# Performance work log

Hardware: AMD Instinct MI355X
Metric: run time of the kernel (lower is better)

The kernel has to match this reference:

```python
import jax, jax.numpy as jnp
import numpy as np

B, S, H = 4, 256, 768
F = 32            # num_features
T = 256           # TAG_HIDDEN_SIZE
WD = 64           # WIDTH_HIDDEN_SIZE
C = 16            # num_tags


def setup_inputs() -> dict:
    key = jax.random.key(0)
    ks = jax.random.split(key, 10)
    inp = {
        "final_hidden": jax.random.normal(ks[0], (B, S, H), jnp.float32),
        "feature_vecs": jax.random.normal(ks[1], (B, S, F), jnp.float32),
        # Linear params stored [in, out] (transposed vs torch; same math)
        "start_W": jax.random.normal(ks[2], (H + F, T), jnp.float32) * (1.0 / np.sqrt(H + F)),
        "start_b": jnp.zeros((T,), jnp.float32),
        "end_W": jax.random.normal(ks[3], (H + F, T), jnp.float32) * (1.0 / np.sqrt(H + F)),
        "end_b": jnp.zeros((T,), jnp.float32),
        "U": jax.random.normal(ks[4], (T, C, T), jnp.float32) * (1.0 / np.sqrt(T)),
        "width_hidden": jax.random.uniform(ks[5], (S, S, WD), jnp.float32),
        "lin_W": jax.random.normal(ks[6], (2 * T + WD, C), jnp.float32) * (1.0 / np.sqrt(2 * T + WD)),
        "lin_b": jnp.zeros((C,), jnp.float32),
    }
    return inp


def reference(final_hidden, feature_vecs, start_W, start_b, end_W, end_b, U, width_hidden, lin_W, lin_b):
    # dropout p=0.0 -> identity
    x = jnp.concatenate([final_hidden, feature_vecs], axis=-1)   # [B,S,H+F]
    s = x @ start_W + start_b                                    # [B,S,T]
    e = x @ end_W + end_b                                        # [B,S,T]

    # biaffine term: einsum('bsh,hci->bsci') then ('bsci,bei->bsec')
    sU = jnp.einsum('bst,tcu->bscu', s, U)                       # [B,S,C,T]
    pre = jnp.einsum('bscu,beu->bsec', sU, e)                    # [B,S,S,C]

    # pairwise FFN, fused: Linear over concat(start, end, width) decomposes
    # into three small matmuls + broadcast adds (same math, no O(S^2*(2T+W)) buffer)
    Ws, We, Ww = lin_W[:T], lin_W[T:2 * T], lin_W[2 * T:]
    ffn = (jnp.einsum('bst,tc->bsc', s, Ws)[:, :, None, :]
           + jnp.einsum('bet,tc->bec', e, We)[:, None, :, :]
           + jnp.einsum('sew,wc->sec', width_hidden, Ww)[None]
           + lin_b)                                              # [B,S,S,C]
    return pre + ffn
```

## Files before the change

kernel.cpp:

```cpp
#include <hip/hip_runtime.h>


#define B_ 4
#define S_ 256
#define H_ 768
#define F_ 32
#define T_ 256
#define C_ 16
#define R_ 1024
#define HF 800
#define HFP 832

typedef unsigned short u16;
typedef __attribute__((ext_vector_type(8))) short short8;
typedef __attribute__((ext_vector_type(4))) float f32x4;

__device__ __forceinline__ u16 f2b(float x) {
    unsigned u = __builtin_bit_cast(unsigned, x);
    u += 0x7FFF + ((u >> 16) & 1);
    return (u16)(u >> 16);
}
__device__ __forceinline__ float b2f(u16 b) {
    unsigned u = ((unsigned)b) << 16;
    return __builtin_bit_cast(float, u);
}

template<int K, int LDA, int LDB, int MF, int NF, int UNROLL>
__device__ __forceinline__ void core(const u16* __restrict__ A,
                                     const u16* __restrict__ B,
                                     int lr, int kgl, f32x4 acc[MF][NF])
{
    const u16* ap[MF];
    const u16* bp[NF];
#pragma unroll
    for (int i = 0; i < MF; ++i) ap[i] = A + (size_t)(i * 16 + lr) * LDA + kgl * 8;
#pragma unroll
    for (int j = 0; j < NF; ++j) bp[j] = B + (size_t)(j * 16 + lr) * LDB + kgl * 8;

#pragma unroll UNROLL
    for (int k = 0; k < K; k += 32) {
        short8 a[MF], b[NF];
#pragma unroll
        for (int i = 0; i < MF; ++i) a[i] = *(const short8*)(ap[i] + k);
#pragma unroll
        for (int j = 0; j < NF; ++j) b[j] = *(const short8*)(bp[j] + k);
#pragma unroll
        for (int i = 0; i < MF; ++i)
#pragma unroll
            for (int j = 0; j < NF; ++j)
                acc[i][j] = __builtin_amdgcn_mfma_f32_16x16x32_bf16(a[i], b[j], acc[i][j], 0, 0, 0);
    }
}

__global__ __launch_bounds__(256)
void k_cvt1(const float* __restrict__ fh, const float* __restrict__ fv,
            const float* __restrict__ sW, const float* __restrict__ eW,
            u16* __restrict__ Xb, u16* __restrict__ Wt)
{
    const int bid = blockIdx.x;
    const int tid = threadIdx.x;

    if (bid < 832) {
        int idx = bid * 256 + tid;
        int r = idx / 208, c4 = idx % 208;
        int k = c4 * 4;
        float4 v;
        if (k < H_)       v = *(const float4*)&fh[r * H_ + k];
        else if (k < HF)  v = *(const float4*)&fv[r * F_ + k - H_];
        else              v = make_float4(0.f, 0.f, 0.f, 0.f);
        ushort4 o; o.x = f2b(v.x); o.y = f2b(v.y); o.z = f2b(v.z); o.w = f2b(v.w);
        *(ushort4*)&Xb[(size_t)r * HFP + k] = o;
    } else if (bid < 1232) {
        __shared__ float t_[32][33];
        int bid2 = bid - 832;
        int k0 = (bid2 / 16) * 32;
        int j0 = (bid2 % 16) * 32;
        const float* src = (j0 < T_) ? sW : eW;
        const int js = (j0 < T_) ? j0 : j0 - T_;
        {
            int jl = tid & 31, kl0 = (tid >> 5) * 4;
#pragma unroll
            for (int i = 0; i < 4; ++i)
                t_[kl0 + i][jl] = src[(k0 + kl0 + i) * T_ + js + jl];
        }
        __syncthreads();
        {
            int kl = tid & 31, jl0 = (tid >> 5) * 4;
#pragma unroll
            for (int i = 0; i < 4; ++i)
                Wt[(size_t)(j0 + jl0 + i) * HFP + k0 + kl] = f2b(t_[kl][jl0 + i]);
        }
    } else {
        int idx = (bid - 1232) * 256 + tid;
        int r = idx >> 3, c4 = idx & 7;
        ushort4 z; z.x = z.y = z.z = z.w = 0;
        *(ushort4*)&Wt[(size_t)r * HFP + HF + c4 * 4] = z;
    }
}

__global__ __launch_bounds__(256)
void k_se_cvtu(const u16* __restrict__ Xb, const u16* __restrict__ Wt,
               const float* __restrict__ sb, const float* __restrict__ eb,
               const float* __restrict__ U,
               u16* __restrict__ SEb, u16* __restrict__ Ut)
{
    const int bid = blockIdx.x;
    const int tid = threadIdx.x;

    if (bid < 256) {
        const int l = tid & 63, w = tid >> 6;
        const int wj = w & 1, wr2 = w >> 1;
        const int lr = l & 15, kgl = l >> 4;
        const int bm = (bid & 15) * 32;
        const int bn = (bid >> 4) * 64;
        f32x4 acc[1][2] = {};

        core<HFP, HFP, HFP, 1, 2, 2>(Wt + (size_t)(bm + wj * 16) * HFP,
                                     Xb + (size_t)(bn + wr2 * 32) * HFP,
                                     lr, kgl, acc);

        int j0 = bm + wj * 16 + kgl * 4;
        float4 bias = (j0 < T_) ? *(const float4*)&sb[j0]
                                : *(const float4*)&eb[j0 - T_];
#pragma unroll
        for (int jj = 0; jj < 2; ++jj) {
            int r = bn + wr2 * 32 + jj * 16 + lr;
            ushort4 o;
            o.x = f2b(acc[0][jj][0] + bias.x);
            o.y = f2b(acc[0][jj][1] + bias.y);
            o.z = f2b(acc[0][jj][2] + bias.z);
            o.w = f2b(acc[0][jj][3] + bias.w);
            *(ushort4*)&SEb[(size_t)r * 512 + j0] = o;
        }
        return;
    }
    {
        __shared__ float t_[32][33];
        int bid2 = bid - 256;
        int cu0 = (bid2 >> 3) * 32;
        int t0  = (bid2 & 7) * 32;
        {
            int cul = tid & 31, tl0 = (tid >> 5) * 4;
#pragma unroll
            for (int i = 0; i < 4; ++i)
                t_[tl0 + i][cul] = U[(size_t)(t0 + tl0 + i) * 4096 + cu0 + cul];
        }
        __syncthreads();
        {
            int tl = tid & 31, cul0 = (tid >> 5) * 4;
#pragma unroll
            for (int i = 0; i < 4; ++i)
                Ut[(size_t)(cu0 + cul0 + i) * T_ + t0 + tl] = f2b(t_[tl][cul0 + i]);
        }
    }
}

__global__ __launch_bounds__(256)
void k_su_scec_wc(const u16* __restrict__ SEb, const u16* __restrict__ Ut,
                  const float* __restrict__ linW, const float* __restrict__ linb,
                  const float* __restrict__ WH,
                  u16* __restrict__ SUb, float* __restrict__ SCEC,
                  float* __restrict__ WC)
{
    const int bid = blockIdx.x;
    const int tid = threadIdx.x;

    if (bid < 512) {
        const int l = tid & 63, w = tid >> 6;
        const int wcu = w & 1, wr2 = w >> 1;
        const int lr = l & 15, kgl = l >> 4;
        const int bm = (bid & 31) * 128;
        const int bn = (bid >> 5) * 64;
        f32x4 acc[4][2] = {};

        core<T_, T_, 512, 4, 2, 2>(Ut + (size_t)(bm + wcu * 64) * T_,
                                   SEb + (size_t)(bn + wr2 * 32) * 512,
                                   lr, kgl, acc);

#pragma unroll
        for (int i = 0; i < 4; ++i) {
            int cu0 = bm + wcu * 64 + i * 16 + kgl * 4;
#pragma unroll
            for (int j = 0; j < 2; ++j) {
                int r = bn + wr2 * 32 + j * 16 + lr;
                ushort4 o;
                o.x = f2b(acc[i][j][0]); o.y = f2b(acc[i][j][1]);
                o.z = f2b(acc[i][j][2]); o.w = f2b(acc[i][j][3]);
                *(ushort4*)&SUb[(size_t)r * 4096 + cu0] = o;
            }
        }
        return;
    }
    if (bid < 768) {
        __shared__ float SEl[4][512];
        const int r0 = (bid - 512) * 4;
#pragma unroll
        for (int i = 0; i < 2; ++i) {
            int ch = tid + i * 256;
            int rl = ch >> 7, o4 = (ch & 127) * 4;
            ushort4 v = *(const ushort4*)&SEb[(size_t)(r0 + rl) * 512 + o4];
            SEl[rl][o4 + 0] = b2f(v.x); SEl[rl][o4 + 1] = b2f(v.y);
            SEl[rl][o4 + 2] = b2f(v.z); SEl[rl][o4 + 3] = b2f(v.w);
        }
        __syncthreads();
        const int rl = tid >> 6, tq = (tid >> 4) & 3, c = tid & 15;
        const int t0 = tq * 64;
        float accs = 0.f, acce = 0.f;
#pragma unroll 4
        for (int t = t0; t < t0 + 64; ++t) {
            accs += SEl[rl][t]       * linW[t * 16 + c];
            acce += SEl[rl][256 + t] * linW[(256 + t) * 16 + c];
        }
        accs += __shfl_xor(accs, 16); accs += __shfl_xor(accs, 32);
        acce += __shfl_xor(acce, 16); acce += __shfl_xor(acce, 32);
        if (tq == 0) {
            SCEC[(r0 + rl) * 32 + c]      = accs;
            SCEC[(r0 + rl) * 32 + 16 + c] = acce;
        }
        return;
    }
    {
        __shared__ float Wl[16][64];
        __shared__ float Wwl[64][16];
        const int se0 = (bid - 768) * 128;
        {
            int w0 = tid >> 2, c4 = tid & 3;
            *(float4*)&Wwl[w0][c4 * 4] = *(const float4*)&linW[(512 + w0) * 16 + c4 * 4];
        }
        const int sel = tid >> 4, c = tid & 15;
        const float lb = linb[c];
#pragma unroll
        for (int it = 0; it < 8; ++it) {
            __syncthreads();
            {
                int w4 = tid & 15;
                *(float4*)&Wl[sel][w4 * 4] =
                    *(const float4*)&WH[(size_t)(se0 + it * 16 + sel) * 64 + w4 * 4];
            }
            __syncthreads();
            float acc = lb;
#pragma unroll
            for (int w0 = 0; w0 < 64; ++w0)
                acc += Wl[sel][w0] * Wwl[w0][c];
            WC[(size_t)(se0 + it * 16 + sel) * 16 + c] = acc;
        }
    }
}

__global__ __launch_bounds__(256)
void k_pre(const u16* __restrict__ SEb, const u16* __restrict__ SUb,
           const float* __restrict__ SCEC, const float* __restrict__ WC,
           float* __restrict__ OUT)
{
    const int bid = blockIdx.x;
    const int tid = threadIdx.x;
    const int b  = bid >> 7;
    const int q2 = bid & 127;
    const int bm = (q2 & 63) * 64;
    const int bn = (q2 >> 6) * 128;
    const int l = tid & 63, w = tid >> 6;
    const int wn = w >> 1, we = w & 1;
    const int lr = l & 15, kgl = l >> 4;
    f32x4 acc[2][4] = {};

    const u16* An = SUb + ((size_t)b << 20) + (size_t)(bm + wn * 32) * T_;
    const u16* Be = SEb + (size_t)(b << 8) * 512 + 256 + (size_t)(bn + we * 64) * 512;

    core<T_, T_, 512, 2, 4, 2>(An, Be, lr, kgl, acc);

    const int c0 = kgl * 4;
#pragma unroll
    for (int i = 0; i < 2; ++i) {
        int n0 = bm + wn * 32 + i * 16;
        int s = n0 >> 4;
        float4 scv = *(const float4*)&SCEC[((b << 8) + s) * 32 + c0];
#pragma unroll
        for (int j = 0; j < 4; ++j) {
            int e = bn + we * 64 + j * 16 + lr;
            float4 ecv = *(const float4*)&SCEC[((b << 8) + e) * 32 + 16 + c0];
            float4 wcv = *(const float4*)&WC[(size_t)(s * S_ + e) * 16 + c0];
            float4 o;
            o.x = acc[i][j][0] + scv.x + ecv.x + wcv.x;
            o.y = acc[i][j][1] + scv.y + ecv.y + wcv.y;
            o.z = acc[i][j][2] + scv.z + ecv.z + wcv.z;
            o.w = acc[i][j][3] + scv.w + ecv.w + wcv.w;
            *(float4*)&OUT[(((size_t)(b << 8) + s) * S_ + e) * 16 + c0] = o;
        }
    }
}

extern "C" void kernel_launch(void* const* d_in, const int* in_sizes, int n_in,
                              void* d_out, int out_size, void* d_ws, size_t ws_size,
                              hipStream_t stream)
{
    const float* fh   = (const float*)d_in[0];
    const float* fv   = (const float*)d_in[1];
    const float* sW   = (const float*)d_in[2];
    const float* sb   = (const float*)d_in[3];
    const float* eW   = (const float*)d_in[4];
    const float* eb   = (const float*)d_in[5];
    const float* U    = (const float*)d_in[6];
    const float* WH   = (const float*)d_in[7];
    const float* linW = (const float*)d_in[8];
    const float* linb = (const float*)d_in[9];
    float* OUT = (float*)d_out;

    char* p = (char*)d_ws;
    u16* SUb = (u16*)p;      p += (size_t)B_ * 4096 * 256 * 2;
    float* WC = (float*)p;   p += (size_t)S_ * S_ * C_ * 4;
    u16* Ut  = (u16*)p;      p += (size_t)4096 * T_ * 2;
    u16* Xb  = (u16*)p;      p += (size_t)R_ * HFP * 2;
    u16* Wt  = (u16*)p;      p += (size_t)512 * HFP * 2;
    u16* SEb = (u16*)p;      p += (size_t)R_ * 512 * 2;
    float* SCEC = (float*)p; p += (size_t)R_ * 32 * 4;

    k_cvt1<<<dim3(1248), 256, 0, stream>>>(fh, fv, sW, eW, Xb, Wt);
    k_se_cvtu<<<dim3(1280), 256, 0, stream>>>(Xb, Wt, sb, eb, U, SEb, Ut);
    k_su_scec_wc<<<dim3(1280), 256, 0, stream>>>(SEb, Ut, linW, linb, WH,
                                                 SUb, SCEC, WC);
    k_pre<<<dim3(512), 256, 0, stream>>>(SEb, SUb, SCEC, WC, OUT);
}
```

Before: 64.27 us.

## Fuse activation bf16 conversion into SE GEMM and rebalance kernel work

The separate activation-to-bf16 pass and its padded Xb buffer are removed. The SE projection GEMM now reads fp32 hidden and feature inputs directly and converts them in registers, using larger 64x64 tiles with the 32 extra features handled as one tail step. The WC width-projection work moves into the second kernel. The SU GEMM gets 128x128 tiles, and k_pre changes its block ordering and unroll depth. This removes one global round-trip of the activations but adds conversion ALU work inside the GEMM loop and cuts the number of SE blocks, which lowers parallelism.

Result: faster. 62.01 us (-3.5%).

```diff
diff --git a/kernel.cpp b/kernel.cpp
--- a/kernel.cpp
+++ b/kernel.cpp
@@ -9,7 +9,6 @@
 #define C_ 16
 #define R_ 1024
 #define HF 800
-#define HFP 832
 
 typedef unsigned short u16;
 typedef __attribute__((ext_vector_type(8))) short short8;
@@ -24,6 +23,14 @@
     unsigned u = ((unsigned)b) << 16;
     return __builtin_bit_cast(float, u);
 }
+__device__ __forceinline__ short8 cvt8(float4 a, float4 b) {
+    short8 r;
+    r[0] = (short)f2b(a.x); r[1] = (short)f2b(a.y);
+    r[2] = (short)f2b(a.z); r[3] = (short)f2b(a.w);
+    r[4] = (short)f2b(b.x); r[5] = (short)f2b(b.y);
+    r[6] = (short)f2b(b.z); r[7] = (short)f2b(b.w);
+    return r;
+}
 
 template<int K, int LDA, int LDB, int MF, int NF, int UNROLL>
 __device__ __forceinline__ void core(const u16* __restrict__ A,
@@ -53,90 +60,106 @@
 }
 
 __global__ __launch_bounds__(256)
-void k_cvt1(const float* __restrict__ fh, const float* __restrict__ fv,
-            const float* __restrict__ sW, const float* __restrict__ eW,
-            u16* __restrict__ Xb, u16* __restrict__ Wt)
-{
+void k_cvtw(const float* __restrict__ sW, const float* __restrict__ eW,
+            u16* __restrict__ Wt)
+{
+    __shared__ float t_[32][33];
     const int bid = blockIdx.x;
     const int tid = threadIdx.x;
-
-    if (bid < 832) {
-        int idx = bid * 256 + tid;
-        int r = idx / 208, c4 = idx % 208;
-        int k = c4 * 4;
-        float4 v;
-        if (k < H_)       v = *(const float4*)&fh[r * H_ + k];
-        else if (k < HF)  v = *(const float4*)&fv[r * F_ + k - H_];
-        else              v = make_float4(0.f, 0.f, 0.f, 0.f);
-        ushort4 o; o.x = f2b(v.x); o.y = f2b(v.y); o.z = f2b(v.z); o.w = f2b(v.w);
-        *(ushort4*)&Xb[(size_t)r * HFP + k] = o;
-    } else if (bid < 1232) {
-        __shared__ float t_[32][33];
-        int bid2 = bid - 832;
-        int k0 = (bid2 / 16) * 32;
-        int j0 = (bid2 % 16) * 32;
-        const float* src = (j0 < T_) ? sW : eW;
-        const int js = (j0 < T_) ? j0 : j0 - T_;
-        {
-            int jl = tid & 31, kl0 = (tid >> 5) * 4;
-#pragma unroll
-            for (int i = 0; i < 4; ++i)
-                t_[kl0 + i][jl] = src[(k0 + kl0 + i) * T_ + js + jl];
-        }
-        __syncthreads();
-        {
-            int kl = tid & 31, jl0 = (tid >> 5) * 4;
-#pragma unroll
-            for (int i = 0; i < 4; ++i)
-                Wt[(size_t)(j0 + jl0 + i) * HFP + k0 + kl] = f2b(t_[kl][jl0 + i]);
-        }
-    } else {
-        int idx = (bid - 1232) * 256 + tid;
-        int r = idx >> 3, c4 = idx & 7;
-        ushort4 z; z.x = z.y = z.z = z.w = 0;
-        *(ushort4*)&Wt[(size_t)r * HFP + HF + c4 * 4] = z;
+    int k0 = (bid / 16) * 32;
+    int j0 = (bid % 16) * 32;
+    const float* src = (j0 < T_) ? sW : eW;
+    const int js = (j0 < T_) ? j0 : j0 - T_;
+    {
+        int jl = tid & 31, kl0 = (tid >> 5) * 4;
+#pragma unroll
+        for (int i = 0; i < 4; ++i)
+            t_[kl0 + i][jl] = src[(k0 + kl0 + i) * T_ + js + jl];
+    }
+    __syncthreads();
+    {
+        int kl = tid & 31, jl0 = (tid >> 5) * 4;
+#pragma unroll
+        for (int i = 0; i < 4; ++i)
+            Wt[(size_t)(j0 + jl0 + i) * HF + k0 + kl] = f2b(t_[kl][jl0 + i]);
     }
 }
 
 __global__ __launch_bounds__(256)
-void k_se_cvtu(const u16* __restrict__ Xb, const u16* __restrict__ Wt,
-               const float* __restrict__ sb, const float* __restrict__ eb,
-               const float* __restrict__ U,
-               u16* __restrict__ SEb, u16* __restrict__ Ut)
+void k_se_cvtu_wc(const float* __restrict__ fh, const float* __restrict__ fv,
+                  const u16* __restrict__ Wt,
+                  const float* __restrict__ sb, const float* __restrict__ eb,
+                  const float* __restrict__ U,
+                  const float* __restrict__ linW, const float* __restrict__ linb,
+                  const float* __restrict__ WH,
+                  u16* __restrict__ SEb, u16* __restrict__ Ut,
+                  float* __restrict__ WC)
 {
     const int bid = blockIdx.x;
     const int tid = threadIdx.x;
 
-    if (bid < 256) {
+    if (bid < 128) {
         const int l = tid & 63, w = tid >> 6;
-        const int wj = w & 1, wr2 = w >> 1;
+        const int wr = w >> 1, wc = w & 1;
         const int lr = l & 15, kgl = l >> 4;
-        const int bm = (bid & 15) * 32;
-        const int bn = (bid >> 4) * 64;
-        f32x4 acc[1][2] = {};
-
-        core<HFP, HFP, HFP, 1, 2, 2>(Wt + (size_t)(bm + wj * 16) * HFP,
-                                     Xb + (size_t)(bn + wr2 * 32) * HFP,
-                                     lr, kgl, acc);
-
-        int j0 = bm + wj * 16 + kgl * 4;
-        float4 bias = (j0 < T_) ? *(const float4*)&sb[j0]
-                                : *(const float4*)&eb[j0 - T_];
-#pragma unroll
-        for (int jj = 0; jj < 2; ++jj) {
-            int r = bn + wr2 * 32 + jj * 16 + lr;
-            ushort4 o;
-            o.x = f2b(acc[0][jj][0] + bias.x);
-            o.y = f2b(acc[0][jj][1] + bias.y);
-            o.z = f2b(acc[0][jj][2] + bias.z);
-            o.w = f2b(acc[0][jj][3] + bias.w);
-            *(ushort4*)&SEb[(size_t)r * 512 + j0] = o;
+        const int bm = (bid >> 4) * 64;
+        const int bn = (bid & 15) * 64;
+        f32x4 acc[2][2] = {};
+
+        const u16* aw0 = Wt + (size_t)(bm + wr * 32 + lr) * HF + kgl * 8;
+        const u16* aw1 = aw0 + (size_t)16 * HF;
+        const float* xr0 = fh + (size_t)(bn + wc * 32 + lr) * H_ + kgl * 8;
+        const float* xr1 = xr0 + (size_t)16 * H_;
+
+#pragma unroll 4
+        for (int k = 0; k < 768; k += 32) {
+            short8 a0 = *(const short8*)(aw0 + k);
+            short8 a1 = *(const short8*)(aw1 + k);
+            float4 p0 = *(const float4*)(xr0 + k);
+            float4 p1 = *(const float4*)(xr0 + k + 4);
+            float4 q0 = *(const float4*)(xr1 + k);
+            float4 q1 = *(const float4*)(xr1 + k + 4);
+            short8 b0 = cvt8(p0, p1);
+            short8 b1 = cvt8(q0, q1);
+            acc[0][0] = __builtin_amdgcn_mfma_f32_16x16x32_bf16(a0, b0, acc[0][0], 0, 0, 0);
+            acc[0][1] = __builtin_amdgcn_mfma_f32_16x16x32_bf16(a0, b1, acc[0][1], 0, 0, 0);
+            acc[1][0] = __builtin_amdgcn_mfma_f32_16x16x32_bf16(a1, b0, acc[1][0], 0, 0, 0);
+            acc[1][1] = __builtin_amdgcn_mfma_f32_16x16x32_bf16(a1, b1, acc[1][1], 0, 0, 0);
+        }
+        {
+            short8 a0 = *(const short8*)(aw0 + 768);
+            short8 a1 = *(const short8*)(aw1 + 768);
+            const float* v0 = fv + (size_t)(bn + wc * 32 + lr) * F_ + kgl * 8;
+            const float* v1 = v0 + (size_t)16 * F_;
+            short8 b0 = cvt8(*(const float4*)v0, *(const float4*)(v0 + 4));
+            short8 b1 = cvt8(*(const float4*)v1, *(const float4*)(v1 + 4));
+            acc[0][0] = __builtin_amdgcn_mfma_f32_16x16x32_bf16(a0, b0, acc[0][0], 0, 0, 0);
+            acc[0][1] = __builtin_amdgcn_mfma_f32_16x16x32_bf16(a0, b1, acc[0][1], 0, 0, 0);
+            acc[1][0] = __builtin_amdgcn_mfma_f32_16x16x32_bf16(a1, b0, acc[1][0], 0, 0, 0);
+            acc[1][1] = __builtin_amdgcn_mfma_f32_16x16x32_bf16(a1, b1, acc[1][1], 0, 0, 0);
+        }
+
+#pragma unroll
+        for (int i = 0; i < 2; ++i) {
+            int j0 = bm + wr * 32 + i * 16 + kgl * 4;
+            float4 bias = (j0 < T_) ? *(const float4*)&sb[j0]
+                                    : *(const float4*)&eb[j0 - T_];
+#pragma unroll
+            for (int jj = 0; jj < 2; ++jj) {
+                int r = bn + wc * 32 + jj * 16 + lr;
+                ushort4 o;
+                o.x = f2b(acc[i][jj][0] + bias.x);
+                o.y = f2b(acc[i][jj][1] + bias.y);
+                o.z = f2b(acc[i][jj][2] + bias.z);
+                o.w = f2b(acc[i][jj][3] + bias.w);
+                *(ushort4*)&SEb[(size_t)r * 512 + j0] = o;
+            }
         }
         return;
     }
-    {
+    if (bid < 1152) {
         __shared__ float t_[32][33];
-        int bid2 = bid - 256;
+        int bid2 = bid - 128;
         int cu0 = (bid2 >> 3) * 32;
         int t0  = (bid2 & 7) * 32;
         {
@@ -152,77 +175,12 @@
             for (int i = 0; i < 4; ++i)
                 Ut[(size_t)(cu0 + cul0 + i) * T_ + t0 + tl] = f2b(t_[tl][cul0 + i]);
         }
-    }
-}
-
-__global__ __launch_bounds__(256)
-void k_su_scec_wc(const u16* __restrict__ SEb, const u16* __restrict__ Ut,
-                  const float* __restrict__ linW, const float* __restrict__ linb,
-                  const float* __restrict__ WH,
-                  u16* __restrict__ SUb, float* __restrict__ SCEC,
-                  float* __restrict__ WC)
-{
-    const int bid = blockIdx.x;
-    const int tid = threadIdx.x;
-
-    if (bid < 512) {
-        const int l = tid & 63, w = tid >> 6;
-        const int wcu = w & 1, wr2 = w >> 1;
-        const int lr = l & 15, kgl = l >> 4;
-        const int bm = (bid & 31) * 128;
-        const int bn = (bid >> 5) * 64;
-        f32x4 acc[4][2] = {};
-
-        core<T_, T_, 512, 4, 2, 2>(Ut + (size_t)(bm + wcu * 64) * T_,
-                                   SEb + (size_t)(bn + wr2 * 32) * 512,
-                                   lr, kgl, acc);
-
-#pragma unroll
-        for (int i = 0; i < 4; ++i) {
-            int cu0 = bm + wcu * 64 + i * 16 + kgl * 4;
-#pragma unroll
-            for (int j = 0; j < 2; ++j) {
-                int r = bn + wr2 * 32 + j * 16 + lr;
-                ushort4 o;
-                o.x = f2b(acc[i][j][0]); o.y = f2b(acc[i][j][1]);
-                o.z = f2b(acc[i][j][2]); o.w = f2b(acc[i][j][3]);
-                *(ushort4*)&SUb[(size_t)r * 4096 + cu0] = o;
-            }
-        }
-        return;
-    }
-    if (bid < 768) {
-        __shared__ float SEl[4][512];
-        const int r0 = (bid - 512) * 4;
-#pragma unroll
-        for (int i = 0; i < 2; ++i) {
-            int ch = tid + i * 256;
-            int rl = ch >> 7, o4 = (ch & 127) * 4;
-            ushort4 v = *(const ushort4*)&SEb[(size_t)(r0 + rl) * 512 + o4];
-            SEl[rl][o4 + 0] = b2f(v.x); SEl[rl][o4 + 1] = b2f(v.y);
-            SEl[rl][o4 + 2] = b2f(v.z); SEl[rl][o4 + 3] = b2f(v.w);
-        }
-        __syncthreads();
-        const int rl = tid >> 6, tq = (tid >> 4) & 3, c = tid & 15;
-        const int t0 = tq * 64;
-        float accs = 0.f, acce = 0.f;
-#pragma unroll 4
-        for (int t = t0; t < t0 + 64; ++t) {
-            accs += SEl[rl][t]       * linW[t * 16 + c];
-            acce += SEl[rl][256 + t] * linW[(256 + t) * 16 + c];
-        }
-        accs += __shfl_xor(accs, 16); accs += __shfl_xor(accs, 32);
-        acce += __shfl_xor(acce, 16); acce += __shfl_xor(acce, 32);
-        if (tq == 0) {
-            SCEC[(r0 + rl) * 32 + c]      = accs;
-            SCEC[(r0 + rl) * 32 + 16 + c] = acce;
-        }
         return;
     }
     {
         __shared__ float Wl[16][64];
         __shared__ float Wwl[64][16];
-        const int se0 = (bid - 768) * 128;
+        const int se0 = (bid - 1152) * 128;
         {
             int w0 = tid >> 2, c4 = tid & 3;
             *(float4*)&Wwl[w0][c4 * 4] = *(const float4*)&linW[(512 + w0) * 16 + c4 * 4];
@@ -248,16 +206,80 @@
 }
 
 __global__ __launch_bounds__(256)
+void k_su_scec(const u16* __restrict__ SEb, const u16* __restrict__ Ut,
+               const float* __restrict__ linW,
+               u16* __restrict__ SUb, float* __restrict__ SCEC)
+{
+    const int bid = blockIdx.x;
+    const int tid = threadIdx.x;
+
+    if (bid < 256) {
+        const int l = tid & 63, w = tid >> 6;
+        const int wcu = w & 1, wr2 = w >> 1;
+        const int lr = l & 15, kgl = l >> 4;
+        const int bm = (bid & 31) * 128;
+        const int bn = (bid >> 5) * 128;
+        f32x4 acc[4][4] = {};
+
+        core<T_, T_, 512, 4, 4, 2>(Ut + (size_t)(bm + wcu * 64) * T_,
+                                   SEb + (size_t)(bn + wr2 * 64) * 512,
+                                   lr, kgl, acc);
+
+#pragma unroll
+        for (int i = 0; i < 4; ++i) {
+            int cu0 = bm + wcu * 64 + i * 16 + kgl * 4;
+#pragma unroll
+            for (int j = 0; j < 4; ++j) {
+                int r = bn + wr2 * 64 + j * 16 + lr;
+                ushort4 o;
+                o.x = f2b(acc[i][j][0]); o.y = f2b(acc[i][j][1]);
+                o.z = f2b(acc[i][j][2]); o.w = f2b(acc[i][j][3]);
+                *(ushort4*)&SUb[(size_t)r * 4096 + cu0] = o;
+            }
+        }
+        return;
+    }
+    {
+        __shared__ float SEl[4][512];
+        const int r0 = (bid - 256) * 4;
+#pragma unroll
+        for (int i = 0; i < 2; ++i) {
+            int ch = tid + i * 256;
+            int rl = ch >> 7, o4 = (ch & 127) * 4;
+            ushort4 v = *(const ushort4*)&SEb[(size_t)(r0 + rl) * 512 + o4];
+            SEl[rl][o4 + 0] = b2f(v.x); SEl[rl][o4 + 1] = b2f(v.y);
+            SEl[rl][o4 + 2] = b2f(v.z); SEl[rl][o4 + 3] = b2f(v.w);
+        }
+        __syncthreads();
+        const int rl = tid >> 6, tq = (tid >> 4) & 3, c = tid & 15;
+        const int t0 = tq * 64;
+        float accs = 0.f, acce = 0.f;
+#pragma unroll 4
+        for (int t = t0; t < t0 + 64; ++t) {
+            accs += SEl[rl][t]       * linW[t * 16 + c];
+            acce += SEl[rl][256 + t] * linW[(256 + t) * 16 + c];
+        }
+        accs += __shfl_xor(accs, 16); accs += __shfl_xor(accs, 32);
+        acce += __shfl_xor(acce, 16); acce += __shfl_xor(acce, 32);
+        if (tq == 0) {
+            SCEC[(r0 + rl) * 32 + c]      = accs;
+            SCEC[(r0 + rl) * 32 + 16 + c] = acce;
+        }
+    }
+}
+
+__global__ __launch_bounds__(256)
 void k_pre(const u16* __restrict__ SEb, const u16* __restrict__ SUb,
            const float* __restrict__ SCEC, const float* __restrict__ WC,
            float* __restrict__ OUT)
 {
     const int bid = blockIdx.x;
     const int tid = threadIdx.x;
-    const int b  = bid >> 7;
-    const int q2 = bid & 127;
-    const int bm = (q2 & 63) * 64;
-    const int bn = (q2 >> 6) * 128;
+    const int n_idx = bid >> 3;
+    const int b  = (bid >> 1) & 3;
+    const int e_idx = bid & 1;
+    const int bm = n_idx * 64;
+    const int bn = e_idx * 128;
     const int l = tid & 63, w = tid >> 6;
     const int wn = w >> 1, we = w & 1;
     const int lr = l & 15, kgl = l >> 4;
@@ -266,7 +288,7 @@
     const u16* An = SUb + ((size_t)b << 20) + (size_t)(bm + wn * 32) * T_;
     const u16* Be = SEb + (size_t)(b << 8) * 512 + 256 + (size_t)(bn + we * 64) * 512;
 
-    core<T_, T_, 512, 2, 4, 2>(An, Be, lr, kgl, acc);
+    core<T_, T_, 512, 2, 4, 4>(An, Be, lr, kgl, acc);
 
     const int c0 = kgl * 4;
 #pragma unroll
@@ -309,14 +331,13 @@
     u16* SUb = (u16*)p;      p += (size_t)B_ * 4096 * 256 * 2;
     float* WC = (float*)p;   p += (size_t)S_ * S_ * C_ * 4;
     u16* Ut  = (u16*)p;      p += (size_t)4096 * T_ * 2;
-    u16* Xb  = (u16*)p;      p += (size_t)R_ * HFP * 2;
-    u16* Wt  = (u16*)p;      p += (size_t)512 * HFP * 2;
+    u16* Wt  = (u16*)p;      p += (size_t)512 * HF * 2;
     u16* SEb = (u16*)p;      p += (size_t)R_ * 512 * 2;
     float* SCEC = (float*)p; p += (size_t)R_ * 32 * 4;
 
-    k_cvt1<<<dim3(1248), 256, 0, stream>>>(fh, fv, sW, eW, Xb, Wt);
-    k_se_cvtu<<<dim3(1280), 256, 0, stream>>>(Xb, Wt, sb, eb, U, SEb, Ut);
-    k_su_scec_wc<<<dim3(1280), 256, 0, stream>>>(SEb, Ut, linW, linb, WH,
-                                                 SUb, SCEC, WC);
+    k_cvtw<<<dim3(400), 256, 0, stream>>>(sW, eW, Wt);
+    k_se_cvtu_wc<<<dim3(1664), 256, 0, stream>>>(fh, fv, Wt, sb, eb, U,
+                                                 linW, linb, WH, SEb, Ut, WC);
+    k_su_scec<<<dim3(512), 256, 0, stream>>>(SEb, Ut, linW, SUb, SCEC);
     k_pre<<<dim3(512), 256, 0, stream>>>(SEb, SUb, SCEC, WC, OUT);
 }
```
